# Kernel optimization log

Hardware: AMD Instinct MI355X
Metric: run time of the kernel (lower is better)

The kernel has to match this reference:

```python
import jax, jax.numpy as jnp
import numpy as np

N = 50000
E = 300000
NEG_SLOPE = 0.2
EPS = 1e-16


def setup_inputs() -> dict:
    key = jax.random.key(0)
    ks = jax.random.split(key, 12)
    x = jax.random.normal(ks[0], (N, 27), dtype=jnp.float32)
    edge_index = jax.random.randint(ks[1], (2, E), 0, N, dtype=jnp.int64)
    # layer 1: in=27 -> heads1=4, dim=64
    W1 = jax.random.normal(ks[2], (27, 4 * 64), dtype=jnp.float32) * 0.1
    a_src1 = jax.random.normal(ks[3], (4, 64), dtype=jnp.float32) * 0.1
    a_dst1 = jax.random.normal(ks[4], (4, 64), dtype=jnp.float32) * 0.1
    b1 = jnp.zeros((4 * 64,), dtype=jnp.float32)
    # layer 2: in=256 -> heads2=2, dim=64
    W2 = jax.random.normal(ks[5], (256, 2 * 64), dtype=jnp.float32) * 0.05
    a_src2 = jax.random.normal(ks[6], (2, 64), dtype=jnp.float32) * 0.1
    a_dst2 = jax.random.normal(ks[7], (2, 64), dtype=jnp.float32) * 0.1
    b2 = jnp.zeros((2 * 64,), dtype=jnp.float32)
    # final linear: 128 -> 1
    Wfc = jax.random.normal(ks[8], (128, 1), dtype=jnp.float32) * 0.05
    bfc = jnp.zeros((1,), dtype=jnp.float32)
    return {"x": x, "edge_index": edge_index, "W1": W1, "a_src1": a_src1,
            "a_dst1": a_dst1, "b1": b1, "W2": W2, "a_src2": a_src2,
            "a_dst2": a_dst2, "b2": b2, "Wfc": Wfc, "bfc": bfc}


def gat_layer(x, src, dst, W, a_src, a_dst, b, heads, dim):
    # h: [N, H, D]
    h = (x @ W).reshape(N, heads, dim)
    # per-node attention half-scores: [N, H]
    s_src = jnp.einsum('nhd,hd->nh', h, a_src)
    s_dst = jnp.einsum('nhd,hd->nh', h, a_dst)
    # per-edge logits (gather) + leaky relu: [E', H]
    logits = jax.nn.leaky_relu(s_src[src] + s_dst[dst], negative_slope=NEG_SLOPE)
    # segment softmax over incoming edges at each destination node
    m = jax.ops.segment_max(logits, dst, num_segments=N)  # [N, H]
    m = jnp.where(jnp.isfinite(m), m, 0.0)
    e = jnp.exp(logits - m[dst])
    z = jax.ops.segment_sum(e, dst, num_segments=N)  # [N, H]
    alpha = e / (z[dst] + EPS)
    # weighted scatter-aggregate of source features
    out = jax.ops.segment_sum(h[src] * alpha[:, :, None], dst, num_segments=N)
    return out.reshape(N, heads * dim) + b


def reference(x, edge_index, W1, a_src1, a_dst1, b1, W2, a_src2, a_dst2, b2, Wfc, bfc):
    # add self-loops (PyG GATConv default add_self_loops=True)
    loops = jnp.arange(N, dtype=edge_index.dtype)
    src = jnp.concatenate([edge_index[0], loops])
    dst = jnp.concatenate([edge_index[1], loops])
    h = gat_layer(x, src, dst, W1, a_src1, a_dst1, b1, heads=4, dim=64)
    h = jax.nn.elu(h)
    h = gat_layer(h, src, dst, W2, a_src2, a_dst2, b2, heads=2, dim=64)
    h = jax.nn.elu(h)
    out = h @ Wfc + bfc
    return jax.nn.sigmoid(out)
```

## Files before the change

### kernel.cpp

```cpp
#include <hip/hip_runtime.h>
#include <math.h>

#define N_NODES 50000
#define N_PAD   50016
#define E_EDGES 300000
#define E_TOT   350000
#define NEG 0.2f
#define EPS 1e-16f
#define CAP 32
#define PLANE (N_PAD * 32)

typedef __attribute__((ext_vector_type(8))) short bf16x8;
typedef __attribute__((ext_vector_type(4))) float f32x4;

__device__ __forceinline__ float leaky(float x) { return x > 0.f ? x : NEG * x; }
__device__ __forceinline__ short f2bf(float v) {
    unsigned u = __float_as_uint(v);
    u += 0x7fffu + ((u >> 16) & 1u);
    return (short)(u >> 16);
}
__device__ __forceinline__ float bflo(unsigned u) { return __uint_as_float(u << 16); }
__device__ __forceinline__ float bfhi(unsigned u) { return __uint_as_float(u & 0xffff0000u); }
__device__ __forceinline__ unsigned bfpack(short a, short b) {
    return (unsigned)(unsigned short)a | ((unsigned)(unsigned short)b << 16);
}

__global__ __launch_bounds__(256) void k_scatter_s1(const int* __restrict__ ei,
        int* __restrict__ cnt, int* __restrict__ eidx,
        const float* __restrict__ x,
        const float* __restrict__ W1, const float* __restrict__ as1,
        const float* __restrict__ ad1, const float* __restrict__ W2,
        float* __restrict__ s1, short* __restrict__ rec,
        short* __restrict__ W1b, short* __restrict__ W2bT) {
    __shared__ float wsvL[216];
    int t = blockIdx.x * 256 + threadIdx.x;
    if (threadIdx.x < 216) {
        int k = threadIdx.x >> 3, j = threadIdx.x & 7;
        const float* av = (j < 4) ? (as1 + j * 64) : (ad1 + (j - 4) * 64);
        const float* wr = W1 + k * 256 + ((j & 3) * 64);
        float s = 0.f;
        #pragma unroll
        for (int d = 0; d < 64; ++d) s += wr[d] * av[d];
        wsvL[threadIdx.x] = s;
    }
    if (t < E_TOT) {
        int s = (t < E_EDGES) ? ei[t] : (t - E_EDGES);
        int d = (t < E_EDGES) ? ei[E_EDGES + t] : (t - E_EDGES);
        int pos = atomicAdd(&cnt[d], 1);
        if (pos < CAP) eidx[d * CAP + pos] = s;
    }
    if (t < 32768) {
        int col = t >> 8, k = t & 255;
        W2bT[t] = f2bf(W2[k * 128 + col]);
    }
    if (t < 8192) {
        int h = t >> 11, col = (t >> 5) & 63, k = t & 31;
        W1b[t] = f2bf(k < 27 ? W1[k * 256 + h * 64 + col] : 0.f);
    }
    __syncthreads();
    if (t < N_NODES * 8) {
        int n = t >> 3, j = t & 7;
        float s = 0.f;
        #pragma unroll
        for (int k = 0; k < 27; ++k) s += x[n * 27 + k] * wsvL[k * 8 + j];
        s1[t] = s;
        if (j < 4) ((float*)rec)[n * 32 + j] = s;
        int c0 = j * 4;
        short p0 = f2bf(c0 + 0 < 27 ? x[n * 27 + c0 + 0] : 0.f);
        short p1 = f2bf(c0 + 1 < 27 ? x[n * 27 + c0 + 1] : 0.f);
        short p2 = f2bf(c0 + 2 < 27 ? x[n * 27 + c0 + 2] : 0.f);
        short p3 = f2bf(c0 + 3 < 27 ? x[n * 27 + c0 + 3] : 0.f);
        uint2 wv;
        wv.x = bfpack(p0, p1);
        wv.y = bfpack(p2, p3);
        *(uint2*)(rec + n * 64 + 8 + c0) = wv;
    }
}

__global__ __launch_bounds__(256) void k_gather1(const int* __restrict__ cnt,
        const int* __restrict__ eidx, const short* __restrict__ rec,
        const float* __restrict__ s1, short* __restrict__ xagg) {
    const float* recf = (const float*)rec;
    int g = threadIdx.x >> 4;
    int q = threadIdx.x & 15;
    int n = blockIdx.x * 16 + g;
    int c2 = 2 * q;
    if (n >= N_NODES) {
        if (n < N_PAD) {
            *(unsigned*)(xagg + 0 * PLANE + n * 32 + c2) = 0u;
            *(unsigned*)(xagg + 1 * PLANE + n * 32 + c2) = 0u;
            *(unsigned*)(xagg + 2 * PLANE + n * 32 + c2) = 0u;
            *(unsigned*)(xagg + 3 * PLANE + n * 32 + c2) = 0u;
        }
        return;
    }
    int beg = n * CAP;
    int espec = eidx[beg + q];
    int deg = min(cnt[n], CAP);
    int myi = (q < deg) ? espec : n;
    float4 sdv = *(const float4*)(s1 + n * 8 + 4);
    float a0 = 0.f, a1 = 0.f, a2 = 0.f, a3 = 0.f;
    float b0 = 0.f, b1v = 0.f, b2v = 0.f, b3 = 0.f;
    float z0 = 0.f, z1 = 0.f, z2 = 0.f, z3 = 0.f;
    float4 svq = *(const float4*)(recf + myi * 32);
    float me0 = __expf(leaky(svq.x + sdv.x));
    float me1 = __expf(leaky(svq.y + sdv.y));
    float me2 = __expf(leaky(svq.z + sdv.z));
    float me3 = __expf(leaky(svq.w + sdv.w));
    int degw = deg;
    degw = max(degw, __shfl_xor(degw, 16));
    degw = max(degw, __shfl_xor(degw, 32));
    if (degw <= 16) {
        int lw = deg - 1;
        for (int i = 0; i < degw; i += 4) {
            bool m0 = i < deg, m1 = (i + 1) < deg;
            bool m2 = (i + 2) < deg, m3 = (i + 3) < deg;
            int j0 = m0 ? i : lw;
            int j1 = m1 ? i + 1 : lw;
            int j2 = m2 ? i + 2 : lw;
            int j3 = m3 ? i + 3 : lw;
            float g0 = m0 ? 1.f : 0.f, g1 = m1 ? 1.f : 0.f;
            float g2 = m2 ? 1.f : 0.f, g3 = m3 ? 1.f : 0.f;
            int s0 = __shfl(myi, j0, 16);
            int s1i = __shfl(myi, j1, 16);
            int s2i = __shfl(myi, j2, 16);
            int s3 = __shfl(myi, j3, 16);
            float e00 = g0 * __shfl(me0, j0, 16);
            float e01 = g0 * __shfl(me1, j0, 16);
            float e02 = g0 * __shfl(me2, j0, 16);
            float e03 = g0 * __shfl(me3, j0, 16);
            float e10 = g1 * __shfl(me0, j1, 16);
            float e11 = g1 * __shfl(me1, j1, 16);
            float e12 = g1 * __shfl(me2, j1, 16);
            float e13 = g1 * __shfl(me3, j1, 16);
            float e20 = g2 * __shfl(me0, j2, 16);
            float e21 = g2 * __shfl(me1, j2, 16);
            float e22 = g2 * __shfl(me2, j2, 16);
            float e23 = g2 * __shfl(me3, j2, 16);
            float e30 = g3 * __shfl(me0, j3, 16);
            float e31 = g3 * __shfl(me1, j3, 16);
            float e32 = g3 * __shfl(me2, j3, 16);
            float e33 = g3 * __shfl(me3, j3, 16);
            unsigned xv0 = *(const unsigned*)(rec + s0 * 64 + 8 + c2);
            unsigned xv1 = *(const unsigned*)(rec + s1i * 64 + 8 + c2);
            unsigned xv2 = *(const unsigned*)(rec + s2i * 64 + 8 + c2);
            unsigned xv3 = *(const unsigned*)(rec + s3 * 64 + 8 + c2);
            float xa0 = bflo(xv0), xc0 = bfhi(xv0);
            float xa1 = bflo(xv1), xc1 = bfhi(xv1);
            float xa2 = bflo(xv2), xc2 = bfhi(xv2);
            float xa3 = bflo(xv3), xc3 = bfhi(xv3);
            z0 += e00 + e10 + e20 + e30;
            z1 += e01 + e11 + e21 + e31;
            z2 += e02 + e12 + e22 + e32;
            z3 += e03 + e13 + e23 + e33;
            a0 += e00 * xa0 + e10 * xa1 + e20 * xa2 + e30 * xa3;
            a1 += e01 * xa0 + e11 * xa1 + e21 * xa2 + e31 * xa3;
            a2 += e02 * xa0 + e12 * xa1 + e22 * xa2 + e32 * xa3;
            a3 += e03 * xa0 + e13 * xa1 + e23 * xa2 + e33 * xa3;
            b0  += e00 * xc0 + e10 * xc1 + e20 * xc2 + e30 * xc3;
            b1v += e01 * xc0 + e11 * xc1 + e21 * xc2 + e31 * xc3;
            b2v += e02 * xc0 + e12 * xc1 + e22 * xc2 + e32 * xc3;
            b3  += e03 * xc0 + e13 * xc1 + e23 * xc2 + e33 * xc3;
        }
    } else {
        int last = beg + deg - 1;
        for (int i = 0; i < deg; i += 4) {
            bool m1 = (i + 1) < deg, m2 = (i + 2) < deg, m3 = (i + 3) < deg;
            int p0 = beg + i;
            int p1 = m1 ? p0 + 1 : last;
            int p2 = m2 ? p0 + 2 : last;
            int p3 = m3 ? p0 + 3 : last;
            int s0 = eidx[p0];
            int s1i = eidx[p1];
            int s2i = eidx[p2];
            int s3 = eidx[p3];
            float4 sv0 = *(const float4*)(recf + s0 * 32);
            float4 sv1 = *(const float4*)(recf + s1i * 32);
            float4 sv2 = *(const float4*)(recf + s2i * 32);
            float4 sv3 = *(const float4*)(recf + s3 * 32);
            unsigned xv0 = *(const unsigned*)(rec + s0 * 64 + 8 + c2);
            unsigned xv1 = *(const unsigned*)(rec + s1i * 64 + 8 + c2);
            unsigned xv2 = *(const unsigned*)(rec + s2i * 64 + 8 + c2);
            unsigned xv3 = *(const unsigned*)(rec + s3 * 64 + 8 + c2);
            float xa0 = bflo(xv0), xc0 = bfhi(xv0);
            float xa1 = bflo(xv1), xc1 = bfhi(xv1);
            float xa2 = bflo(xv2), xc2 = bfhi(xv2);
            float xa3 = bflo(xv3), xc3 = bfhi(xv3);
            float g1 = m1 ? 1.f : 0.f, g2 = m2 ? 1.f : 0.f, g3 = m3 ? 1.f : 0.f;
            float e00 = __expf(leaky(sv0.x + sdv.x));
            float e01 = __expf(leaky(sv0.y + sdv.y));
            float e02 = __expf(leaky(sv0.z + sdv.z));
            float e03 = __expf(leaky(sv0.w + sdv.w));
            float e10 = g1 * __expf(leaky(sv1.x + sdv.x));
            float e11 = g1 * __expf(leaky(sv1.y + sdv.y));
            float e12 = g1 * __expf(leaky(sv1.z + sdv.z));
            float e13 = g1 * __expf(leaky(sv1.w + sdv.w));
            float e20 = g2 * __expf(leaky(sv2.x + sdv.x));
            float e21 = g2 * __expf(leaky(sv2.y + sdv.y));
            float e22 = g2 * __expf(leaky(sv2.z + sdv.z));
            float e23 = g2 * __expf(leaky(sv2.w + sdv.w));
            float e30 = g3 * __expf(leaky(sv3.x + sdv.x));
            float e31 = g3 * __expf(leaky(sv3.y + sdv.y));
            float e32 = g3 * __expf(leaky(sv3.z + sdv.z));
            float e33 = g3 * __expf(leaky(sv3.w + sdv.w));
            z0 += e00 + e10 + e20 + e30;
            z1 += e01 + e11 + e21 + e31;
            z2 += e02 + e12 + e22 + e32;
            z3 += e03 + e13 + e23 + e33;
            a0 += e00 * xa0 + e10 * xa1 + e20 * xa2 + e30 * xa3;
            a1 += e01 * xa0 + e11 * xa1 + e21 * xa2 + e31 * xa3;
            a2 += e02 * xa0 + e12 * xa1 + e22 * xa2 + e32 * xa3;
            a3 += e03 * xa0 + e13 * xa1 + e23 * xa2 + e33 * xa3;
            b0  += e00 * xc0 + e10 * xc1 + e20 * xc2 + e30 * xc3;
            b1v += e01 * xc0 + e11 * xc1 + e21 * xc2 + e31 * xc3;
            b2v += e02 * xc0 + e12 * xc1 + e22 * xc2 + e32 * xc3;
            b3  += e03 * xc0 + e13 * xc1 + e23 * xc2 + e33 * xc3;
        }
    }
    float i0 = 1.f / (z0 + EPS), i1 = 1.f / (z1 + EPS);
    float i2 = 1.f / (z2 + EPS), i3 = 1.f / (z3 + EPS);
    *(unsigned*)(xagg + 0 * PLANE + n * 32 + c2) = bfpack(f2bf(a0 * i0), f2bf(b0 * i0));
    *(unsigned*)(xagg + 1 * PLANE + n * 32 + c2) = bfpack(f2bf(a1 * i1), f2bf(b1v * i1));
    *(unsigned*)(xagg + 2 * PLANE + n * 32 + c2) = bfpack(f2bf(a2 * i2), f2bf(b2v * i2));
    *(unsigned*)(xagg + 3 * PLANE + n * 32 + c2) = bfpack(f2bf(a3 * i3), f2bf(b3 * i3));
}

__global__ __launch_bounds__(256) void k_dense(const short* __restrict__ xagg,
        const short* __restrict__ W1b, const short* __restrict__ W2bT,
        const float* __restrict__ b1, const float* __restrict__ as2,
        const float* __restrict__ ad2, short* __restrict__ h2b,
        float* __restrict__ s2) {
    __shared__ short O[32 * 264];
    __shared__ float P[4][2][32];
    int w = threadIdx.x >> 6, l = threadIdx.x & 63;
    int lane16 = l & 15, quad = l >> 4;
    int n0 = blockIdx.x * 32;
    f32x4 z4 = {0.f, 0.f, 0.f, 0.f};

    {
        bf16x8 am0 = *(const bf16x8*)&xagg[w * PLANE + (n0 + lane16) * 32 + quad * 8];
        bf16x8 am1 = *(const bf16x8*)&xagg[w * PLANE + (n0 + 16 + lane16) * 32 + quad * 8];
        f32x4 c0[4], c1[4];
        #pragma unroll
        for (int nt = 0; nt < 4; ++nt) {
            bf16x8 b = *(const bf16x8*)&W1b[w * 2048 + (nt * 16 + lane16) * 32 + quad * 8];
            c0[nt] = __builtin_amdgcn_mfma_f32_16x16x32_bf16(am0, b, z4, 0, 0, 0);
            c1[nt] = __builtin_amdgcn_mfma_f32_16x16x32_bf16(am1, b, z4, 0, 0, 0);
        }
        #pragma unroll
        for (int nt = 0; nt < 4; ++nt) {
            int col = w * 64 + nt * 16 + lane16;
            float bb = b1[col];
            #pragma unroll
            for (int r2 = 0; r2 < 4; ++r2) {
                float v = c0[nt][r2] + bb;
                v = v > 0.f ? v : __expf(v) - 1.f;
                O[(quad * 4 + r2) * 264 + col] = f2bf(v);
                float u = c1[nt][r2] + bb;
                u = u > 0.f ? u : __expf(u) - 1.f;
                O[(16 + quad * 4 + r2) * 264 + col] = f2bf(u);
            }
        }
    }
    __syncthreads();

    f32x4 acc[2][2];
    acc[0][0] = z4; acc[0][1] = z4; acc[1][0] = z4; acc[1][1] = z4;
    for (int k0 = 0; k0 < 256; k0 += 32) {
        bf16x8 a0 = *(const bf16x8*)&O[lane16 * 264 + k0 + quad * 8];
        bf16x8 a1 = *(const bf16x8*)&O[(16 + lane16) * 264 + k0 + quad * 8];
        #pragma unroll
        for (int j = 0; j < 2; ++j) {
            int ct = 2 * w + j;
            bf16x8 b2 = *(const bf16x8*)&W2bT[(ct * 16 + lane16) * 256 + k0 + quad * 8];
            acc[0][j] = __builtin_amdgcn_mfma_f32_16x16x32_bf16(a0, b2, acc[0][j], 0, 0, 0);
            acc[1][j] = __builtin_amdgcn_mfma_f32_16x16x32_bf16(a1, b2, acc[1][j], 0, 0, 0);
        }
    }
    float ps[2][4] = {{0.f,0.f,0.f,0.f},{0.f,0.f,0.f,0.f}};
    float pd[2][4] = {{0.f,0.f,0.f,0.f},{0.f,0.f,0.f,0.f}};
    #pragma unroll
    for (int j = 0; j < 2; ++j) {
        int col = (2 * w + j) * 16 + lane16;
        float a_s = as2[col], a_d = ad2[col];
        #pragma unroll
        for (int m = 0; m < 2; ++m) {
            #pragma unroll
            for (int r2 = 0; r2 < 4; ++r2) {
                ps[m][r2] += acc[m][j][r2] * a_s;
                pd[m][r2] += acc[m][j][r2] * a_d;
                int row = n0 + m * 16 + quad * 4 + r2;
                if (row < N_NODES) h2b[row * 128 + col] = f2bf(acc[m][j][r2]);
            }
        }
    }
    #pragma unroll
    for (int off = 1; off <= 8; off <<= 1)
        #pragma unroll
        for (int m = 0; m < 2; ++m)
            #pragma unroll
            for (int r2 = 0; r2 < 4; ++r2) {
                ps[m][r2] += __shfl_xor(ps[m][r2], off);
                pd[m][r2] += __shfl_xor(pd[m][r2], off);
            }
    if (lane16 == 0) {
        #pragma unroll
        for (int m = 0; m < 2; ++m)
            #pragma unroll
            for (int r2 = 0; r2 < 4; ++r2) {
                P[w][0][m * 16 + quad * 4 + r2] = ps[m][r2];
                P[w][1][m * 16 + quad * 4 + r2] = pd[m][r2];
            }
    }
    __syncthreads();
    if (threadIdx.x < 64) {
        int m = threadIdx.x & 31, hd = threadIdx.x >> 5;
        int row = n0 + m;
        if (row < N_NODES) {
            s2[row * 4 + hd]     = P[2 * hd][0][m] + P[2 * hd + 1][0][m];
            s2[row * 4 + 2 + hd] = P[2 * hd][1][m] + P[2 * hd + 1][1][m];
        }
    }
}

__global__ __launch_bounds__(256) void k_agg2_csr(const int* __restrict__ cnt,
        const int* __restrict__ eidx, const float* __restrict__ s2,
        const short* __restrict__ h2b, const float* __restrict__ b2,
        const float* __restrict__ Wfc, const float* __restrict__ bfc,
        float* __restrict__ out) {
    int g = threadIdx.x >> 4;
    int q = threadIdx.x & 15;
    int n = blockIdx.x * 16 + g;
    int beg = n * CAP;
    int espec = eidx[beg + q];
    int deg = min(cnt[n], CAP);
    int myi = (q < deg) ? espec : n;
    int h = q >> 3;
    float2 sdv = *(const float2*)(s2 + n * 4 + 2);
    float4 accA = make_float4(0.f, 0.f, 0.f, 0.f);
    float4 accB = make_float4(0.f, 0.f, 0.f, 0.f);
    float z = 0.f;
    float2 svq = *(const float2*)(s2 + myi * 4);
    float mea = __expf(leaky(svq.x + sdv.x));
    float meb = __expf(leaky(svq.y + sdv.y));
    int degw = deg;
    degw = max(degw, __shfl_xor(degw, 16));
    degw = max(degw, __shfl_xor(degw, 32));
    if (degw <= 16) {
        int lw = deg - 1;
        for (int i = 0; i < degw; i += 4) {
            bool m0 = i < deg, m1 = (i + 1) < deg;
            bool m2 = (i + 2) < deg, m3 = (i + 3) < deg;
            int j0 = m0 ? i : lw;
            int j1 = m1 ? i + 1 : lw;
            int j2 = m2 ? i + 2 : lw;
            int j3 = m3 ? i + 3 : lw;
            int a0 = __shfl(myi, j0, 16);
            int a1 = __shfl(myi, j1, 16);
            int a2 = __shfl(myi, j2, 16);
            int a3 = __shfl(myi, j3, 16);
            float ea0 = __shfl(mea, j0, 16), eb0 = __shfl(meb, j0, 16);
            float ea1 = __shfl(mea, j1, 16), eb1 = __shfl(meb, j1, 16);
            float ea2 = __shfl(mea, j2, 16), eb2 = __shfl(meb, j2, 16);
            float ea3 = __shfl(mea, j3, 16), eb3 = __shfl(meb, j3, 16);
            float e0 = (m0 ? 1.f : 0.f) * (h ? eb0 : ea0);
            float e1 = (m1 ? 1.f : 0.f) * (h ? eb1 : ea1);
            float e2 = (m2 ? 1.f : 0.f) * (h ? eb2 : ea2);
            float e3 = (m3 ? 1.f : 0.f) * (h ? eb3 : ea3);
            uint4 v0 = *(const uint4*)(h2b + a0 * 128 + q * 8);
            uint4 v1 = *(const uint4*)(h2b + a1 * 128 + q * 8);
            uint4 v2 = *(const uint4*)(h2b + a2 * 128 + q * 8);
            uint4 v3 = *(const uint4*)(h2b + a3 * 128 + q * 8);
            z += e0 + e1 + e2 + e3;
            accA.x += e0 * bflo(v0.x) + e1 * bflo(v1.x) + e2 * bflo(v2.x) + e3 * bflo(v3.x);
            accA.y += e0 * bfhi(v0.x) + e1 * bfhi(v1.x) + e2 * bfhi(v2.x) + e3 * bfhi(v3.x);
            accA.z += e0 * bflo(v0.y) + e1 * bflo(v1.y) + e2 * bflo(v2.y) + e3 * bflo(v3.y);
            accA.w += e0 * bfhi(v0.y) + e1 * bfhi(v1.y) + e2 * bfhi(v2.y) + e3 * bfhi(v3.y);
            accB.x += e0 * bflo(v0.z) + e1 * bflo(v1.z) + e2 * bflo(v2.z) + e3 * bflo(v3.z);
            accB.y += e0 * bfhi(v0.z) + e1 * bfhi(v1.z) + e2 * bfhi(v2.z) + e3 * bfhi(v3.z);
            accB.z += e0 * bflo(v0.w) + e1 * bflo(v1.w) + e2 * bflo(v2.w) + e3 * bflo(v3.w);
            accB.w += e0 * bfhi(v0.w) + e1 * bfhi(v1.w) + e2 * bfhi(v2.w) + e3 * bfhi(v3.w);
        }
    } else {
        float sd = h ? sdv.y : sdv.x;
        int i = 0;
        for (; i + 4 <= deg; i += 4) {
            int a0 = eidx[beg + i], a1 = eidx[beg + i + 1];
            int a2 = eidx[beg + i + 2], a3 = eidx[beg + i + 3];
            float e0 = __expf(leaky(s2[a0 * 4 + h] + sd));
            float e1 = __expf(leaky(s2[a1 * 4 + h] + sd));
            float e2 = __expf(leaky(s2[a2 * 4 + h] + sd));
            float e3 = __expf(leaky(s2[a3 * 4 + h] + sd));
            uint4 v0 = *(const uint4*)(h2b + a0 * 128 + q * 8);
            uint4 v1 = *(const uint4*)(h2b + a1 * 128 + q * 8);
            uint4 v2 = *(const uint4*)(h2b + a2 * 128 + q * 8);
            uint4 v3 = *(const uint4*)(h2b + a3 * 128 + q * 8);
            z += e0 + e1 + e2 + e3;
            accA.x += e0 * bflo(v0.x) + e1 * bflo(v1.x) + e2 * bflo(v2.x) + e3 * bflo(v3.x);
            accA.y += e0 * bfhi(v0.x) + e1 * bfhi(v1.x) + e2 * bfhi(v2.x) + e3 * bfhi(v3.x);
            accA.z += e0 * bflo(v0.y) + e1 * bflo(v1.y) + e2 * bflo(v2.y) + e3 * bflo(v3.y);
            accA.w += e0 * bfhi(v0.y) + e1 * bfhi(v1.y) + e2 * bfhi(v2.y) + e3 * bfhi(v3.y);
            accB.x += e0 * bflo(v0.z) + e1 * bflo(v1.z) + e2 * bflo(v2.z) + e3 * bflo(v3.z);
            accB.y += e0 * bfhi(v0.z) + e1 * bfhi(v1.z) + e2 * bfhi(v2.z) + e3 * bfhi(v3.z);
            accB.z += e0 * bflo(v0.w) + e1 * bflo(v1.w) + e2 * bflo(v2.w) + e3 * bflo(v3.w);
            accB.w += e0 * bfhi(v0.w) + e1 * bfhi(v1.w) + e2 * bfhi(v2.w) + e3 * bfhi(v3.w);
        }
        for (; i < deg; ++i) {
            int a0 = eidx[beg + i];
            float e0 = __expf(leaky(s2[a0 * 4 + h] + sd));
            uint4 v0 = *(const uint4*)(h2b + a0 * 128 + q * 8);
            z += e0;
            accA.x += e0 * bflo(v0.x); accA.y += e0 * bfhi(v0.x);
            accA.z += e0 * bflo(v0.y); accA.w += e0 * bfhi(v0.y);
            accB.x += e0 * bflo(v0.z); accB.y += e0 * bfhi(v0.z);
            accB.z += e0 * bflo(v0.w); accB.w += e0 * bfhi(v0.w);
        }
    }
    float inv = 1.f / (z + EPS);
    int c0 = q * 8;
    float p = 0.f;
    float va[8] = {accA.x, accA.y, accA.z, accA.w, accB.x, accB.y, accB.z, accB.w};
    #pragma unroll
    for (int j = 0; j < 8; ++j) {
        float v = va[j] * inv + b2[c0 + j];
        v = v > 0.f ? v : __expf(v) - 1.f;
        p += v * Wfc[c0 + j];
    }
    #pragma unroll
    for (int off = 1; off <= 8; off <<= 1) p += __shfl_xor(p, off);
    if (q == 0) out[n] = 1.f / (1.f + __expf(-(p + bfc[0])));
}

extern "C" void kernel_launch(void* const* d_in, const int* in_sizes, int n_in,
                              void* d_out, int out_size, void* d_ws, size_t ws_size,
                              hipStream_t stream) {
    const float* x   = (const float*)d_in[0];
    const int*   ei  = (const int*)d_in[1];
    const float* W1  = (const float*)d_in[2];
    const float* as1 = (const float*)d_in[3];
    const float* ad1 = (const float*)d_in[4];
    const float* b1  = (const float*)d_in[5];
    const float* W2  = (const float*)d_in[6];
    const float* as2 = (const float*)d_in[7];
    const float* ad2 = (const float*)d_in[8];
    const float* b2  = (const float*)d_in[9];
    const float* Wfc = (const float*)d_in[10];
    const float* bfc = (const float*)d_in[11];
    float* out = (float*)d_out;

    float* f = (float*)d_ws;
    short* h2b   = (short*)f;
    float* s1    = f + 3200000;
    float* s2    = f + 3600000;
    int*   cnt   = (int*)(f + 3810000);
    int*   eidx  = (int*)(f + 3870000);
    short* W1b   = (short*)(f + 5500000);
    short* W2bT  = (short*)(f + 5510000);
    short* xagg  = (short*)(f + 6400000);
    short* rec   = (short*)(f + 9700000);

    hipMemsetAsync(cnt, 0, N_NODES * sizeof(int), stream);

    k_scatter_s1<<<1563, 256, 0, stream>>>(ei, cnt, eidx, x, W1, as1, ad1, W2,
                                           s1, rec, W1b, W2bT);

    k_gather1<<<3126, 256, 0, stream>>>(cnt, eidx, rec, s1, xagg);

    k_dense<<<1563, 256, 0, stream>>>(xagg, W1b, W2bT, b1, as2, ad2, h2b, s2);

    k_agg2_csr<<<3125, 256, 0, stream>>>(cnt, eidx, s2, h2b, b2, Wfc, bfc, out);
}
```

Before: 166.6 us.

## Fuse layer-1 gather aggregation into dense MFMA kernel via shared memory

```diff
diff --git a/kernel.cpp b/kernel.cpp
--- a/kernel.cpp
+++ b/kernel.cpp
@@ -8,7 +8,6 @@
 #define NEG 0.2f
 #define EPS 1e-16f
 #define CAP 32
-#define PLANE (N_PAD * 32)
 
 typedef __attribute__((ext_vector_type(8))) short bf16x8;
 typedef __attribute__((ext_vector_type(4))) float f32x4;
@@ -77,169 +76,172 @@
     }
 }
 
-__global__ __launch_bounds__(256) void k_gather1(const int* __restrict__ cnt,
+__global__ __launch_bounds__(256) void k_gd(const int* __restrict__ cnt,
         const int* __restrict__ eidx, const short* __restrict__ rec,
-        const float* __restrict__ s1, short* __restrict__ xagg) {
-    const float* recf = (const float*)rec;
-    int g = threadIdx.x >> 4;
-    int q = threadIdx.x & 15;
-    int n = blockIdx.x * 16 + g;
-    int c2 = 2 * q;
-    if (n >= N_NODES) {
-        if (n < N_PAD) {
-            *(unsigned*)(xagg + 0 * PLANE + n * 32 + c2) = 0u;
-            *(unsigned*)(xagg + 1 * PLANE + n * 32 + c2) = 0u;
-            *(unsigned*)(xagg + 2 * PLANE + n * 32 + c2) = 0u;
-            *(unsigned*)(xagg + 3 * PLANE + n * 32 + c2) = 0u;
-        }
-        return;
-    }
-    int beg = n * CAP;
-    int espec = eidx[beg + q];
-    int deg = min(cnt[n], CAP);
-    int myi = (q < deg) ? espec : n;
-    float4 sdv = *(const float4*)(s1 + n * 8 + 4);
-    float a0 = 0.f, a1 = 0.f, a2 = 0.f, a3 = 0.f;
-    float b0 = 0.f, b1v = 0.f, b2v = 0.f, b3 = 0.f;
-    float z0 = 0.f, z1 = 0.f, z2 = 0.f, z3 = 0.f;
-    float4 svq = *(const float4*)(recf + myi * 32);
-    float me0 = __expf(leaky(svq.x + sdv.x));
-    float me1 = __expf(leaky(svq.y + sdv.y));
-    float me2 = __expf(leaky(svq.z + sdv.z));
-    float me3 = __expf(leaky(svq.w + sdv.w));
-    int degw = deg;
-    degw = max(degw, __shfl_xor(degw, 16));
-    degw = max(degw, __shfl_xor(degw, 32));
-    if (degw <= 16) {
-        int lw = deg - 1;
-        for (int i = 0; i < degw; i += 4) {
-            bool m0 = i < deg, m1 = (i + 1) < deg;
-            bool m2 = (i + 2) < deg, m3 = (i + 3) < deg;
-            int j0 = m0 ? i : lw;
-            int j1 = m1 ? i + 1 : lw;
-            int j2 = m2 ? i + 2 : lw;
-            int j3 = m3 ? i + 3 : lw;
-            float g0 = m0 ? 1.f : 0.f, g1 = m1 ? 1.f : 0.f;
-            float g2 = m2 ? 1.f : 0.f, g3 = m3 ? 1.f : 0.f;
-            int s0 = __shfl(myi, j0, 16);
-            int s1i = __shfl(myi, j1, 16);
-            int s2i = __shfl(myi, j2, 16);
-            int s3 = __shfl(myi, j3, 16);
-            float e00 = g0 * __shfl(me0, j0, 16);
-            float e01 = g0 * __shfl(me1, j0, 16);
-            float e02 = g0 * __shfl(me2, j0, 16);
-            float e03 = g0 * __shfl(me3, j0, 16);
-            float e10 = g1 * __shfl(me0, j1, 16);
-            float e11 = g1 * __shfl(me1, j1, 16);
-            float e12 = g1 * __shfl(me2, j1, 16);
-            float e13 = g1 * __shfl(me3, j1, 16);
-            float e20 = g2 * __shfl(me0, j2, 16);
-            float e21 = g2 * __shfl(me1, j2, 16);
-            float e22 = g2 * __shfl(me2, j2, 16);
-            float e23 = g2 * __shfl(me3, j2, 16);
-            float e30 = g3 * __shfl(me0, j3, 16);
-            float e31 = g3 * __shfl(me1, j3, 16);
-            float e32 = g3 * __shfl(me2, j3, 16);
-            float e33 = g3 * __shfl(me3, j3, 16);
-            unsigned xv0 = *(const unsigned*)(rec + s0 * 64 + 8 + c2);
-            unsigned xv1 = *(const unsigned*)(rec + s1i * 64 + 8 + c2);
-            unsigned xv2 = *(const unsigned*)(rec + s2i * 64 + 8 + c2);
-            unsigned xv3 = *(const unsigned*)(rec + s3 * 64 + 8 + c2);
-            float xa0 = bflo(xv0), xc0 = bfhi(xv0);
-            float xa1 = bflo(xv1), xc1 = bfhi(xv1);
-            float xa2 = bflo(xv2), xc2 = bfhi(xv2);
-            float xa3 = bflo(xv3), xc3 = bfhi(xv3);
-            z0 += e00 + e10 + e20 + e30;
-            z1 += e01 + e11 + e21 + e31;
-            z2 += e02 + e12 + e22 + e32;
-            z3 += e03 + e13 + e23 + e33;
-            a0 += e00 * xa0 + e10 * xa1 + e20 * xa2 + e30 * xa3;
-            a1 += e01 * xa0 + e11 * xa1 + e21 * xa2 + e31 * xa3;
-            a2 += e02 * xa0 + e12 * xa1 + e22 * xa2 + e32 * xa3;
-            a3 += e03 * xa0 + e13 * xa1 + e23 * xa2 + e33 * xa3;
-            b0  += e00 * xc0 + e10 * xc1 + e20 * xc2 + e30 * xc3;
-            b1v += e01 * xc0 + e11 * xc1 + e21 * xc2 + e31 * xc3;
-            b2v += e02 * xc0 + e12 * xc1 + e22 * xc2 + e32 * xc3;
-            b3  += e03 * xc0 + e13 * xc1 + e23 * xc2 + e33 * xc3;
-        }
-    } else {
-        int last = beg + deg - 1;
-        for (int i = 0; i < deg; i += 4) {
-            bool m1 = (i + 1) < deg, m2 = (i + 2) < deg, m3 = (i + 3) < deg;
-            int p0 = beg + i;
-            int p1 = m1 ? p0 + 1 : last;
-            int p2 = m2 ? p0 + 2 : last;
-            int p3 = m3 ? p0 + 3 : last;
-            int s0 = eidx[p0];
-            int s1i = eidx[p1];
-            int s2i = eidx[p2];
-            int s3 = eidx[p3];
-            float4 sv0 = *(const float4*)(recf + s0 * 32);
-            float4 sv1 = *(const float4*)(recf + s1i * 32);
-            float4 sv2 = *(const float4*)(recf + s2i * 32);
-            float4 sv3 = *(const float4*)(recf + s3 * 32);
-            unsigned xv0 = *(const unsigned*)(rec + s0 * 64 + 8 + c2);
-            unsigned xv1 = *(const unsigned*)(rec + s1i * 64 + 8 + c2);
-            unsigned xv2 = *(const unsigned*)(rec + s2i * 64 + 8 + c2);
-            unsigned xv3 = *(const unsigned*)(rec + s3 * 64 + 8 + c2);
-            float xa0 = bflo(xv0), xc0 = bfhi(xv0);
-            float xa1 = bflo(xv1), xc1 = bfhi(xv1);
-            float xa2 = bflo(xv2), xc2 = bfhi(xv2);
-            float xa3 = bflo(xv3), xc3 = bfhi(xv3);
-            float g1 = m1 ? 1.f : 0.f, g2 = m2 ? 1.f : 0.f, g3 = m3 ? 1.f : 0.f;
-            float e00 = __expf(leaky(sv0.x + sdv.x));
-            float e01 = __expf(leaky(sv0.y + sdv.y));
-            float e02 = __expf(leaky(sv0.z + sdv.z));
-            float e03 = __expf(leaky(sv0.w + sdv.w));
-            float e10 = g1 * __expf(leaky(sv1.x + sdv.x));
-            float e11 = g1 * __expf(leaky(sv1.y + sdv.y));
-            float e12 = g1 * __expf(leaky(sv1.z + sdv.z));
-            float e13 = g1 * __expf(leaky(sv1.w + sdv.w));
-            float e20 = g2 * __expf(leaky(sv2.x + sdv.x));
-            float e21 = g2 * __expf(leaky(sv2.y + sdv.y));
-            float e22 = g2 * __expf(leaky(sv2.z + sdv.z));
-            float e23 = g2 * __expf(leaky(sv2.w + sdv.w));
-            float e30 = g3 * __expf(leaky(sv3.x + sdv.x));
-            float e31 = g3 * __expf(leaky(sv3.y + sdv.y));
-            float e32 = g3 * __expf(leaky(sv3.z + sdv.z));
-            float e33 = g3 * __expf(leaky(sv3.w + sdv.w));
-            z0 += e00 + e10 + e20 + e30;
-            z1 += e01 + e11 + e21 + e31;
-            z2 += e02 + e12 + e22 + e32;
-            z3 += e03 + e13 + e23 + e33;
-            a0 += e00 * xa0 + e10 * xa1 + e20 * xa2 + e30 * xa3;
-            a1 += e01 * xa0 + e11 * xa1 + e21 * xa2 + e31 * xa3;
-            a2 += e02 * xa0 + e12 * xa1 + e22 * xa2 + e32 * xa3;
-            a3 += e03 * xa0 + e13 * xa1 + e23 * xa2 + e33 * xa3;
-            b0  += e00 * xc0 + e10 * xc1 + e20 * xc2 + e30 * xc3;
-            b1v += e01 * xc0 + e11 * xc1 + e21 * xc2 + e31 * xc3;
-            b2v += e02 * xc0 + e12 * xc1 + e22 * xc2 + e32 * xc3;
-            b3  += e03 * xc0 + e13 * xc1 + e23 * xc2 + e33 * xc3;
-        }
-    }
-    float i0 = 1.f / (z0 + EPS), i1 = 1.f / (z1 + EPS);
-    float i2 = 1.f / (z2 + EPS), i3 = 1.f / (z3 + EPS);
-    *(unsigned*)(xagg + 0 * PLANE + n * 32 + c2) = bfpack(f2bf(a0 * i0), f2bf(b0 * i0));
-    *(unsigned*)(xagg + 1 * PLANE + n * 32 + c2) = bfpack(f2bf(a1 * i1), f2bf(b1v * i1));
-    *(unsigned*)(xagg + 2 * PLANE + n * 32 + c2) = bfpack(f2bf(a2 * i2), f2bf(b2v * i2));
-    *(unsigned*)(xagg + 3 * PLANE + n * 32 + c2) = bfpack(f2bf(a3 * i3), f2bf(b3 * i3));
-}
-
-__global__ __launch_bounds__(256) void k_dense(const short* __restrict__ xagg,
-        const short* __restrict__ W1b, const short* __restrict__ W2bT,
-        const float* __restrict__ b1, const float* __restrict__ as2,
-        const float* __restrict__ ad2, short* __restrict__ h2b,
-        float* __restrict__ s2) {
+        const float* __restrict__ s1, const short* __restrict__ W1b,
+        const short* __restrict__ W2bT, const float* __restrict__ b1,
+        const float* __restrict__ as2, const float* __restrict__ ad2,
+        short* __restrict__ h2b, float* __restrict__ s2) {
+    __shared__ short XA[4][32][32];
     __shared__ short O[32 * 264];
     __shared__ float P[4][2][32];
+    const float* recf = (const float*)rec;
+    int n0 = blockIdx.x * 32;
+    f32x4 z4 = {0.f, 0.f, 0.f, 0.f};
+
+    {
+        int g = threadIdx.x >> 4;
+        int q = threadIdx.x & 15;
+        int c2 = 2 * q;
+        #pragma unroll
+        for (int p = 0; p < 2; ++p) {
+            int m = p * 16 + g;
+            int n = n0 + m;
+            if (n >= N_NODES) {
+                *(unsigned*)&XA[0][m][c2] = 0u;
+                *(unsigned*)&XA[1][m][c2] = 0u;
+                *(unsigned*)&XA[2][m][c2] = 0u;
+                *(unsigned*)&XA[3][m][c2] = 0u;
+                continue;
+            }
+            int beg = n * CAP;
+            int espec = eidx[beg + q];
+            int deg = min(cnt[n], CAP);
+            int myi = (q < deg) ? espec : n;
+            float4 sdv = *(const float4*)(s1 + n * 8 + 4);
+            float a0 = 0.f, a1 = 0.f, a2 = 0.f, a3 = 0.f;
+            float b0 = 0.f, b1v = 0.f, b2v = 0.f, b3 = 0.f;
+            float z0 = 0.f, z1 = 0.f, z2 = 0.f, z3 = 0.f;
+            float4 svq = *(const float4*)(recf + myi * 32);
+            float me0 = __expf(leaky(svq.x + sdv.x));
+            float me1 = __expf(leaky(svq.y + sdv.y));
+            float me2 = __expf(leaky(svq.z + sdv.z));
+            float me3 = __expf(leaky(svq.w + sdv.w));
+            int degw = deg;
+            degw = max(degw, __shfl_xor(degw, 16));
+            degw = max(degw, __shfl_xor(degw, 32));
+            if (degw <= 16) {
+                int lw = deg - 1;
+                for (int i = 0; i < degw; i += 4) {
+                    bool m0 = i < deg, m1 = (i + 1) < deg;
+                    bool m2 = (i + 2) < deg, m3 = (i + 3) < deg;
+                    int j0 = m0 ? i : lw;
+                    int j1 = m1 ? i + 1 : lw;
+                    int j2 = m2 ? i + 2 : lw;
+                    int j3 = m3 ? i + 3 : lw;
+                    float g0 = m0 ? 1.f : 0.f, g1 = m1 ? 1.f : 0.f;
+                    float g2 = m2 ? 1.f : 0.f, g3 = m3 ? 1.f : 0.f;
+                    int s0 = __shfl(myi, j0, 16);
+                    int s1i = __shfl(myi, j1, 16);
+                    int s2i = __shfl(myi, j2, 16);
+                    int s3 = __shfl(myi, j3, 16);
+                    float e00 = g0 * __shfl(me0, j0, 16);
+                    float e01 = g0 * __shfl(me1, j0, 16);
+                    float e02 = g0 * __shfl(me2, j0, 16);
+                    float e03 = g0 * __shfl(me3, j0, 16);
+                    float e10 = g1 * __shfl(me0, j1, 16);
+                    float e11 = g1 * __shfl(me1, j1, 16);
+                    float e12 = g1 * __shfl(me2, j1, 16);
+                    float e13 = g1 * __shfl(me3, j1, 16);
+                    float e20 = g2 * __shfl(me0, j2, 16);
+                    float e21 = g2 * __shfl(me1, j2, 16);
+                    float e22 = g2 * __shfl(me2, j2, 16);
+                    float e23 = g2 * __shfl(me3, j2, 16);
+                    float e30 = g3 * __shfl(me0, j3, 16);
+                    float e31 = g3 * __shfl(me1, j3, 16);
+                    float e32 = g3 * __shfl(me2, j3, 16);
+                    float e33 = g3 * __shfl(me3, j3, 16);
+                    unsigned xv0 = *(const unsigned*)(rec + s0 * 64 + 8 + c2);
+                    unsigned xv1 = *(const unsigned*)(rec + s1i * 64 + 8 + c2);
+                    unsigned xv2 = *(const unsigned*)(rec + s2i * 64 + 8 + c2);
+                    unsigned xv3 = *(const unsigned*)(rec + s3 * 64 + 8 + c2);
+                    float xa0 = bflo(xv0), xc0 = bfhi(xv0);
+                    float xa1 = bflo(xv1), xc1 = bfhi(xv1);
+                    float xa2 = bflo(xv2), xc2 = bfhi(xv2);
+                    float xa3 = bflo(xv3), xc3 = bfhi(xv3);
+                    z0 += e00 + e10 + e20 + e30;
+                    z1 += e01 + e11 + e21 + e31;
+                    z2 += e02 + e12 + e22 + e32;
+                    z3 += e03 + e13 + e23 + e33;
+                    a0 += e00 * xa0 + e10 * xa1 + e20 * xa2 + e30 * xa3;
+                    a1 += e01 * xa0 + e11 * xa1 + e21 * xa2 + e31 * xa3;
+                    a2 += e02 * xa0 + e12 * xa1 + e22 * xa2 + e32 * xa3;
+                    a3 += e03 * xa0 + e13 * xa1 + e23 * xa2 + e33 * xa3;
+                    b0  += e00 * xc0 + e10 * xc1 + e20 * xc2 + e30 * xc3;
+                    b1v += e01 * xc0 + e11 * xc1 + e21 * xc2 + e31 * xc3;
+                    b2v += e02 * xc0 + e12 * xc1 + e22 * xc2 + e32 * xc3;
+                    b3  += e03 * xc0 + e13 * xc1 + e23 * xc2 + e33 * xc3;
+                }
+            } else {
+                int last = beg + deg - 1;
+                for (int i = 0; i < deg; i += 4) {
+                    bool m1 = (i + 1) < deg, m2 = (i + 2) < deg, m3 = (i + 3) < deg;
+                    int p0 = beg + i;
+                    int p1 = m1 ? p0 + 1 : last;
+                    int p2 = m2 ? p0 + 2 : last;
+                    int p3 = m3 ? p0 + 3 : last;
+                    int s0 = eidx[p0];
+                    int s1i = eidx[p1];
+                    int s2i = eidx[p2];
+                    int s3 = eidx[p3];
+                    float4 sv0 = *(const float4*)(recf + s0 * 32);
+                    float4 sv1 = *(const float4*)(recf + s1i * 32);
+                    float4 sv2 = *(const float4*)(recf + s2i * 32);
+                    float4 sv3 = *(const float4*)(recf + s3 * 32);
+                    unsigned xv0 = *(const unsigned*)(rec + s0 * 64 + 8 + c2);
+                    unsigned xv1 = *(const unsigned*)(rec + s1i * 64 + 8 + c2);
+                    unsigned xv2 = *(const unsigned*)(rec + s2i * 64 + 8 + c2);
+                    unsigned xv3 = *(const unsigned*)(rec + s3 * 64 + 8 + c2);
+                    float xa0 = bflo(xv0), xc0 = bfhi(xv0);
+                    float xa1 = bflo(xv1), xc1 = bfhi(xv1);
+                    float xa2 = bflo(xv2), xc2 = bfhi(xv2);
+                    float xa3 = bflo(xv3), xc3 = bfhi(xv3);
+                    float g1 = m1 ? 1.f : 0.f, g2 = m2 ? 1.f : 0.f, g3 = m3 ? 1.f : 0.f;
+                    float e00 = __expf(leaky(sv0.x + sdv.x));
+                    float e01 = __expf(leaky(sv0.y + sdv.y));
+                    float e02 = __expf(leaky(sv0.z + sdv.z));
+                    float e03 = __expf(leaky(sv0.w + sdv.w));
+                    float e10 = g1 * __expf(leaky(sv1.x + sdv.x));
+                    float e11 = g1 * __expf(leaky(sv1.y + sdv.y));
+                    float e12 = g1 * __expf(leaky(sv1.z + sdv.z));
+                    float e13 = g1 * __expf(leaky(sv1.w + sdv.w));
+                    float e20 = g2 * __expf(leaky(sv2.x + sdv.x));
+                    float e21 = g2 * __expf(leaky(sv2.y + sdv.y));
+                    float e22 = g2 * __expf(leaky(sv2.z + sdv.z));
+                    float e23 = g2 * __expf(leaky(sv2.w + sdv.w));
+                    float e30 = g3 * __expf(leaky(sv3.x + sdv.x));
+                    float e31 = g3 * __expf(leaky(sv3.y + sdv.y));
+                    float e32 = g3 * __expf(leaky(sv3.z + sdv.z));
+                    float e33 = g3 * __expf(leaky(sv3.w + sdv.w));
+                    z0 += e00 + e10 + e20 + e30;
+                    z1 += e01 + e11 + e21 + e31;
+                    z2 += e02 + e12 + e22 + e32;
+                    z3 += e03 + e13 + e23 + e33;
+                    a0 += e00 * xa0 + e10 * xa1 + e20 * xa2 + e30 * xa3;
+                    a1 += e01 * xa0 + e11 * xa1 + e21 * xa2 + e31 * xa3;
+                    a2 += e02 * xa0 + e12 * xa1 + e22 * xa2 + e32 * xa3;
+                    a3 += e03 * xa0 + e13 * xa1 + e23 * xa2 + e33 * xa3;
+                    b0  += e00 * xc0 + e10 * xc1 + e20 * xc2 + e30 * xc3;
+                    b1v += e01 * xc0 + e11 * xc1 + e21 * xc2 + e31 * xc3;
+                    b2v += e02 * xc0 + e12 * xc1 + e22 * xc2 + e32 * xc3;
+                    b3  += e03 * xc0 + e13 * xc1 + e23 * xc2 + e33 * xc3;
+                }
+            }
+            float i0 = 1.f / (z0 + EPS), i1 = 1.f / (z1 + EPS);
+            float i2 = 1.f / (z2 + EPS), i3 = 1.f / (z3 + EPS);
+            *(unsigned*)&XA[0][m][c2] = bfpack(f2bf(a0 * i0), f2bf(b0 * i0));
+            *(unsigned*)&XA[1][m][c2] = bfpack(f2bf(a1 * i1), f2bf(b1v * i1));
+            *(unsigned*)&XA[2][m][c2] = bfpack(f2bf(a2 * i2), f2bf(b2v * i2));
+            *(unsigned*)&XA[3][m][c2] = bfpack(f2bf(a3 * i3), f2bf(b3 * i3));
+        }
+    }
+    __syncthreads();
+
     int w = threadIdx.x >> 6, l = threadIdx.x & 63;
     int lane16 = l & 15, quad = l >> 4;
-    int n0 = blockIdx.x * 32;
-    f32x4 z4 = {0.f, 0.f, 0.f, 0.f};
-
     {
-        bf16x8 am0 = *(const bf16x8*)&xagg[w * PLANE + (n0 + lane16) * 32 + quad * 8];
-        bf16x8 am1 = *(const bf16x8*)&xagg[w * PLANE + (n0 + 16 + lane16) * 32 + quad * 8];
+        bf16x8 am0 = *(const bf16x8*)&XA[w][lane16][quad * 8];
+        bf16x8 am1 = *(const bf16x8*)&XA[w][16 + lane16][quad * 8];
         f32x4 c0[4], c1[4];
         #pragma unroll
         for (int nt = 0; nt < 4; ++nt) {
@@ -264,6 +266,7 @@
     }
     __syncthreads();
 
+    int n0b = n0;
     f32x4 acc[2][2];
     acc[0][0] = z4; acc[0][1] = z4; acc[1][0] = z4; acc[1][1] = z4;
     for (int k0 = 0; k0 < 256; k0 += 32) {
@@ -289,7 +292,7 @@
             for (int r2 = 0; r2 < 4; ++r2) {
                 ps[m][r2] += acc[m][j][r2] * a_s;
                 pd[m][r2] += acc[m][j][r2] * a_d;
-                int row = n0 + m * 16 + quad * 4 + r2;
+                int row = n0b + m * 16 + quad * 4 + r2;
                 if (row < N_NODES) h2b[row * 128 + col] = f2bf(acc[m][j][r2]);
             }
         }
@@ -315,7 +318,7 @@
     __syncthreads();
     if (threadIdx.x < 64) {
         int m = threadIdx.x & 31, hd = threadIdx.x >> 5;
-        int row = n0 + m;
+        int row = n0b + m;
         if (row < N_NODES) {
             s2[row * 4 + hd]     = P[2 * hd][0][m] + P[2 * hd + 1][0][m];
             s2[row * 4 + 2 + hd] = P[2 * hd][1][m] + P[2 * hd + 1][1][m];
@@ -456,7 +459,6 @@
     int*   eidx  = (int*)(f + 3870000);
     short* W1b   = (short*)(f + 5500000);
     short* W2bT  = (short*)(f + 5510000);
-    short* xagg  = (short*)(f + 6400000);
     short* rec   = (short*)(f + 9700000);
 
     hipMemsetAsync(cnt, 0, N_NODES * sizeof(int), stream);
@@ -464,9 +466,8 @@
     k_scatter_s1<<<1563, 256, 0, stream>>>(ei, cnt, eidx, x, W1, as1, ad1, W2,
                                            s1, rec, W1b, W2bT);
 
-    k_gather1<<<3126, 256, 0, stream>>>(cnt, eidx, rec, s1, xagg);
-
-    k_dense<<<1563, 256, 0, stream>>>(xagg, W1b, W2bT, b1, as2, ad2, h2b, s2);
+    k_gd<<<1563, 256, 0, stream>>>(cnt, eidx, rec, s1, W1b, W2bT, b1,
+                                   as2, ad2, h2b, s2);
 
     k_agg2_csr<<<3125, 256, 0, stream>>>(cnt, eidx, s2, h2b, b2, Wfc, bfc, out);
 }
```

New measurement: 163.9 us, median of 2. No clear change (-1.7%).
